# Kernel optimization log

Hardware: AMD Instinct MI355X
Metric: run time of the kernel (lower is better)

The kernel has to match this reference:

```python
import jax, jax.numpy as jnp
import numpy as np

B, T, C, HS = 32, 2048, 256, 64
LARGE_NEG = -1e9


def setup_inputs() -> dict:
    key = jax.random.key(0)
    k1, k2, k3, k4, k5 = jax.random.split(key, 5)
    q_input = jax.random.normal(k1, (B, T, C), dtype=jnp.float32)
    attn_mask = jax.random.randint(k2, (B, T), 0, 2) > 0  # (B, Tk) bool padding mask
    s = 1.0 / np.sqrt(C)  # ~ nn.Linear default init scale
    Wq = jax.random.normal(k3, (C, HS), dtype=jnp.float32) * s
    Wk = jax.random.normal(k4, (C, HS), dtype=jnp.float32) * s
    Wv = jax.random.normal(k5, (C, HS), dtype=jnp.float32) * s
    return {"q_input": q_input, "Wq": Wq, "Wk": Wk, "Wv": Wv, "attn_mask": attn_mask}


def reference(q_input, Wq, Wk, Wv, attn_mask):
    # self-attention: kv_input = q_input
    q = q_input @ Wq  # (B, Tq, HS)
    k = q_input @ Wk  # (B, Tk, HS)
    v = q_input @ Wv  # (B, Tk, HS)
    scale = HS ** -0.5
    w = jnp.einsum('bqd,bkd->bqk', q, k) * scale  # (B, Tq, Tk)
    causal = jnp.tril(jnp.ones((T, T), dtype=bool))  # tril buffer slice
    w = jnp.where(causal[None, :, :], w, LARGE_NEG)
    # (B, Tk) padding mask -> broadcast over query dim, matching unsqueeze(1)
    w = jnp.where(attn_mask[:, None, :], w, LARGE_NEG)
    w = jax.nn.softmax(w, axis=-1)
    # dropout is identity in eval mode (deterministic reference)
    out = jnp.einsum('bqk,bkd->bqd', w, v)  # (B, Tq, HS)
    return out
```

## Files before the change

kernel.cpp:

```cpp
#include <hip/hip_runtime.h>
#include <hip/hip_bf16.h>

#define NB 32
#define NT 2048
#define NC 256
#define NH 64
#define QB 64
#define KB 64
#define MT 128
#define KC 64

typedef __attribute__((ext_vector_type(8))) short bf16x8;
typedef __attribute__((ext_vector_type(4))) float f32x4;

static constexpr float SCALE2 = 0.18033688011112042f;
static constexpr float LNEG   = -1e9f;

static __device__ inline short f2b(float x) {
    __hip_bfloat16 h = __float2bfloat16(x);
    return *reinterpret_cast<short*>(&h);
}
static __device__ inline float b2f(short s) {
    unsigned int u = ((unsigned int)(unsigned short)s) << 16;
    float f; __builtin_memcpy(&f, &u, 4); return f;
}

static __device__ inline void dma16(const __hip_bfloat16* g, __hip_bfloat16* l) {
    __builtin_amdgcn_global_load_lds(
        (const __attribute__((address_space(1))) unsigned int*)g,
        (__attribute__((address_space(3))) unsigned int*)l, 16, 0, 0);
}

__global__ __launch_bounds__(256) void prep_kernel(
    const float* __restrict__ Wq, const float* __restrict__ Wk,
    const float* __restrict__ Wv, const int* __restrict__ M,
    __hip_bfloat16* __restrict__ Wt, float* __restrict__ Bias)
{
    const int n = blockIdx.x;
    if (n < 192) {
        const int k = threadIdx.x;
        const float* Wm = (n < 64) ? Wq : ((n < 128) ? Wk : Wv);
        Wt[n * NC + k] = __float2bfloat16(Wm[k * NH + (n & 63)]);
    } else {
        const int i = (n - 192) * 256 + threadIdx.x;
        Bias[i] = M[i] ? 0.f : LNEG;
    }
}

__global__ __launch_bounds__(256, 2) void qkv_kernel(
    const float* __restrict__ X, const __hip_bfloat16* __restrict__ Wt,
    __hip_bfloat16* __restrict__ Q, __hip_bfloat16* __restrict__ K,
    __hip_bfloat16* __restrict__ Vt)
{
    __shared__ __hip_bfloat16 x_lds[MT][KC + 8];
    __shared__ __hip_bfloat16 w_lds[192][KC + 8];

    const int row0 = blockIdx.x * MT;
    const int tid  = threadIdx.x;
    const int wid  = tid >> 6;
    const int lane = tid & 63;
    const int l15  = lane & 15;
    const int lg   = lane >> 4;

    f32x4 aQ[4][2], aK[4][2], aV[2][4];
    #pragma unroll
    for (int i = 0; i < 4; ++i)
        #pragma unroll
        for (int j = 0; j < 2; ++j) {
            aQ[i][j] = (f32x4){0.f,0.f,0.f,0.f};
            aK[i][j] = (f32x4){0.f,0.f,0.f,0.f};
            aV[j][i] = (f32x4){0.f,0.f,0.f,0.f};
        }

    float4 xp[4][2];
    bf16x8 wp[6];
    #pragma unroll
    for (int i = 0; i < 4; ++i) {
        int u = tid + i * 256;
        int r = u >> 3, c8 = (u & 7) * 8;
        const float* src = &X[(size_t)(row0 + r) * NC + c8];
        xp[i][0] = *(const float4*)(src);
        xp[i][1] = *(const float4*)(src + 4);
    }
    #pragma unroll
    for (int i = 0; i < 6; ++i) {
        int u = tid + i * 256;
        int r = u >> 3, c8 = (u & 7) * 8;
        wp[i] = *reinterpret_cast<const bf16x8*>(&Wt[r * NC + c8]);
    }

    for (int kc = 0; kc < NC / KC; ++kc) {
        __syncthreads();
        #pragma unroll
        for (int i = 0; i < 4; ++i) {
            int u = tid + i * 256;
            int r = u >> 3, c8 = (u & 7) * 8;
            bf16x8 o;
            o[0]=f2b(xp[i][0].x); o[1]=f2b(xp[i][0].y);
            o[2]=f2b(xp[i][0].z); o[3]=f2b(xp[i][0].w);
            o[4]=f2b(xp[i][1].x); o[5]=f2b(xp[i][1].y);
            o[6]=f2b(xp[i][1].z); o[7]=f2b(xp[i][1].w);
            *reinterpret_cast<bf16x8*>(&x_lds[r][c8]) = o;
        }
        #pragma unroll
        for (int i = 0; i < 6; ++i) {
            int u = tid + i * 256;
            int r = u >> 3, c8 = (u & 7) * 8;
            *reinterpret_cast<bf16x8*>(&w_lds[r][c8]) = wp[i];
        }
        __syncthreads();

        if (kc + 1 < NC / KC) {
            const int off = (kc + 1) * KC;
            #pragma unroll
            for (int i = 0; i < 4; ++i) {
                int u = tid + i * 256;
                int r = u >> 3, c8 = (u & 7) * 8;
                const float* src = &X[(size_t)(row0 + r) * NC + off + c8];
                xp[i][0] = *(const float4*)(src);
                xp[i][1] = *(const float4*)(src + 4);
            }
            #pragma unroll
            for (int i = 0; i < 6; ++i) {
                int u = tid + i * 256;
                int r = u >> 3, c8 = (u & 7) * 8;
                wp[i] = *reinterpret_cast<const bf16x8*>(&Wt[r * NC + off + c8]);
            }
        }

        #pragma unroll
        for (int ks = 0; ks < 2; ++ks) {
            bf16x8 xf[2];
            #pragma unroll
            for (int tf = 0; tf < 2; ++tf)
                xf[tf] = *reinterpret_cast<const bf16x8*>(
                    &x_lds[wid * 32 + tf * 16 + l15][ks * 32 + lg * 8]);
            #pragma unroll
            for (int nf = 0; nf < 4; ++nf) {
                bf16x8 wq = *reinterpret_cast<const bf16x8*>(
                    &w_lds[nf * 16 + l15][ks * 32 + lg * 8]);
                bf16x8 wk = *reinterpret_cast<const bf16x8*>(
                    &w_lds[64 + nf * 16 + l15][ks * 32 + lg * 8]);
                bf16x8 wv = *reinterpret_cast<const bf16x8*>(
                    &w_lds[128 + nf * 16 + l15][ks * 32 + lg * 8]);
                #pragma unroll
                for (int tf = 0; tf < 2; ++tf) {
                    aQ[nf][tf] = __builtin_amdgcn_mfma_f32_16x16x32_bf16(wq, xf[tf], aQ[nf][tf], 0, 0, 0);
                    aK[nf][tf] = __builtin_amdgcn_mfma_f32_16x16x32_bf16(wk, xf[tf], aK[nf][tf], 0, 0, 0);
                    aV[tf][nf] = __builtin_amdgcn_mfma_f32_16x16x32_bf16(xf[tf], wv, aV[tf][nf], 0, 0, 0);
                }
            }
        }
    }

    const int b  = row0 >> 11;
    const int t0 = row0 & (NT - 1);
    #pragma unroll
    for (int nf = 0; nf < 4; ++nf)
        #pragma unroll
        for (int tf = 0; tf < 2; ++tf) {
            size_t o = (size_t)(row0 + wid * 32 + tf * 16 + l15) * NH + nf * 16 + lg * 4;
            short4 sq, sk;
            sq.x = f2b(aQ[nf][tf][0] * SCALE2); sq.y = f2b(aQ[nf][tf][1] * SCALE2);
            sq.z = f2b(aQ[nf][tf][2] * SCALE2); sq.w = f2b(aQ[nf][tf][3] * SCALE2);
            sk.x = f2b(aK[nf][tf][0]); sk.y = f2b(aK[nf][tf][1]);
            sk.z = f2b(aK[nf][tf][2]); sk.w = f2b(aK[nf][tf][3]);
            *reinterpret_cast<short4*>(&Q[o]) = sq;
            *reinterpret_cast<short4*>(&K[o]) = sk;
        }
    #pragma unroll
    for (int tf = 0; tf < 2; ++tf)
        #pragma unroll
        for (int df = 0; df < 4; ++df) {
            int d  = df * 16 + l15;
            int t4 = t0 + wid * 32 + tf * 16 + lg * 4;
            short4 sv;
            sv.x = f2b(aV[tf][df][0]); sv.y = f2b(aV[tf][df][1]);
            sv.z = f2b(aV[tf][df][2]); sv.w = f2b(aV[tf][df][3]);
            *reinterpret_cast<short4*>(&Vt[((size_t)b * NH + d) * NT + t4]) = sv;
        }
}

__global__ __launch_bounds__(1024) void meanv_kernel(
    const __hip_bfloat16* __restrict__ Vt, float* __restrict__ MV)
{
    __shared__ float red[NH][17];
    const int b    = blockIdx.x;
    const int tid  = threadIdx.x;
    const int d    = tid >> 4;
    const int part = tid & 15;
    const __hip_bfloat16* row = Vt + ((size_t)b * NH + d) * NT;
    float s = 0.f;
    for (int t = part * 128; t < part * 128 + 128; t += 8) {
        bf16x8 v = *reinterpret_cast<const bf16x8*>(&row[t]);
        #pragma unroll
        for (int j = 0; j < 8; ++j) s += b2f(v[j]);
    }
    red[d][part] = s;
    __syncthreads();
    if (part == 0) {
        float tot = 0.f;
        #pragma unroll
        for (int i = 0; i < 16; ++i) tot += red[d][i];
        MV[b * NH + d] = tot * (1.0f / NT);
    }
}

template<bool CAUSAL>
static __device__ inline void sm_step(
    int q, int k0, const int (&koff)[4],
    const f32x4 (&s)[4], float& m_r, float& l_r,
    bool& resc, float& al, bf16x8& pb0, bf16x8& pb1)
{
    float y[4][4];
    #pragma unroll
    for (int jt = 0; jt < 4; ++jt)
        #pragma unroll
        for (int r = 0; r < 4; ++r) {
            float v = s[jt][r];
            if (CAUSAL && (k0 + koff[jt] + r > q)) v = LNEG;
            y[jt][r] = v;
        }
    float pmax = y[0][0];
    #pragma unroll
    for (int jt = 0; jt < 4; ++jt)
        #pragma unroll
        for (int r = 0; r < 4; ++r) pmax = fmaxf(pmax, y[jt][r]);

    resc = __any(pmax > m_r + 8.0f);
    al   = 1.0f;
    if (resc) {
        float tm = fmaxf(pmax, __shfl_xor(pmax, 16));
        tm = fmaxf(tm, __shfl_xor(tm, 32));
        const float mnew = fmaxf(m_r, tm);
        al  = __builtin_amdgcn_exp2f(m_r - mnew);
        m_r = mnew;
        l_r *= al;
    }

    float p[4][4], rs = 0.f;
    #pragma unroll
    for (int jt = 0; jt < 4; ++jt)
        #pragma unroll
        for (int r = 0; r < 4; ++r) {
            p[jt][r] = __builtin_amdgcn_exp2f(y[jt][r] - m_r);
            rs += p[jt][r];
        }
    l_r += rs;
    #pragma unroll
    for (int r = 0; r < 4; ++r) {
        pb0[r]     = f2b(p[0][r]);
        pb0[4 + r] = f2b(p[1][r]);
        pb1[r]     = f2b(p[2][r]);
        pb1[4 + r] = f2b(p[3][r]);
    }
}

__global__ __launch_bounds__(256) void attn_kernel(
    const __hip_bfloat16* __restrict__ Q, const __hip_bfloat16* __restrict__ K,
    const __hip_bfloat16* __restrict__ Vt, const float* __restrict__ Bias,
    const float* __restrict__ MV, float* __restrict__ Out)
{
    __shared__ __hip_bfloat16 k_lds[2][KB][NH];
    __shared__ __hip_bfloat16 vt_lds[2][NH][KB];

    const int bid  = blockIdx.x;
    const int xcd  = bid & 7;
    const int slot = bid >> 3;
    const int b    = xcd * 4 + (slot >> 4);
    const int pi   = slot & 15;
    const int gA   = pi, gB = 31 - pi;

    const int tid  = threadIdx.x;
    const int wid  = tid >> 6;
    const int lane = tid & 63;
    const int l15  = lane & 15;
    const int lg   = lane >> 4;

    const __hip_bfloat16* Kg = K  + (size_t)b * NT * NH;
    const __hip_bfloat16* Vg = Vt + (size_t)b * NH * NT;
    const float* Bb = Bias + b * NT;

    const int qA = gA * QB + wid * 16 + l15;
    const int qB = gB * QB + wid * 16 + l15;
    bf16x8 qA0, qA1, qB0, qB1;
    {
        const __hip_bfloat16* Qr = Q + ((size_t)b * NT + qA) * NH;
        qA0 = *reinterpret_cast<const bf16x8*>(&Qr[lg * 8]);
        qA1 = *reinterpret_cast<const bf16x8*>(&Qr[lg * 8 + 32]);
        const __hip_bfloat16* Qs = Q + ((size_t)b * NT + qB) * NH;
        qB0 = *reinterpret_cast<const bf16x8*>(&Qs[lg * 8]);
        qB1 = *reinterpret_cast<const bf16x8*>(&Qs[lg * 8 + 32]);
    }

    f32x4 oA[4], oB[4];
    #pragma unroll
    for (int dt = 0; dt < 4; ++dt) {
        oA[dt] = (f32x4){0.f,0.f,0.f,0.f};
        oB[dt] = (f32x4){0.f,0.f,0.f,0.f};
    }
    float mA = -3.0e38f, lA = 0.f, mB = -3.0e38f, lB = 0.f;

    int kr[4], koff[4];
    #pragma unroll
    for (int jt = 0; jt < 4; ++jt) {
        kr[jt]   = ((jt & 2) << 4) | ((l15 >> 2) << 3) | ((jt & 1) << 2) | (l15 & 3);
        koff[jt] = ((jt & 2) << 4) | (lg << 3) | ((jt & 1) << 2);
    }
    const int swk  = (l15 & 3) | (((l15 >> 2) & 1) << 2);
    const int swv  = (l15 & 3) | (((l15 >> 3) & 1) << 2);
    const int kch0 = ((lg ^ swk) & 7) * 8;
    const int vch0 = ((lg ^ swv) & 7) * 8;

    int srowL[2], schL[2];
    #pragma unroll
    for (int i = 0; i < 2; ++i) {
        const int ci  = wid * 2 + i;
        srowL[i] = ci * 8 + (lane >> 3);
        const int sw = ((lane >> 3) & 3) | ((ci & 1) << 2);
        schL[i]  = ((lane & 7) ^ sw) * 8;
    }

    #define STAGE(buf, kt_) do {                                              \
        const int _k0 = (kt_) * KB;                                           \
        _Pragma("unroll")                                                     \
        for (int i = 0; i < 2; ++i) {                                         \
            dma16(Kg + (size_t)(_k0 + srowL[i]) * NH + schL[i],               \
                  &k_lds[buf][(wid * 2 + i) * 8][0]);                         \
            dma16(Vg + (size_t)srowL[i] * NT + _k0 + schL[i],                 \
                  &vt_lds[buf][(wid * 2 + i) * 8][0]);                        \
        }                                                                     \
    } while (0)

    STAGE(0, 0);
    int cur = 0;

    f32x4 bias_cur[4], bias_nxt[4];
    #pragma unroll
    for (int jt = 0; jt < 4; ++jt)
        bias_cur[jt] = *reinterpret_cast<const f32x4*>(&Bb[koff[jt]]);

    for (int kt = 0; kt <= gB; ++kt) {
        asm volatile("s_waitcnt vmcnt(0)" ::: "memory");
        __syncthreads();
        if (kt < gB) {
            STAGE(cur ^ 1, kt + 1);
            const int kn = (kt + 1) * KB;
            #pragma unroll
            for (int jt = 0; jt < 4; ++jt)
                bias_nxt[jt] = *reinterpret_cast<const f32x4*>(&Bb[kn + koff[jt]]);
        }

        const int k0   = kt * KB;
        const bool aAct = (kt <= gA);

        f32x4 sA[4], sB[4];
        __builtin_amdgcn_s_setprio(1);
        #pragma unroll
        for (int jt = 0; jt < 4; ++jt) {
            bf16x8 kfa = *reinterpret_cast<const bf16x8*>(&k_lds[cur][kr[jt]][kch0]);
            bf16x8 kfb = *reinterpret_cast<const bf16x8*>(&k_lds[cur][kr[jt]][kch0 ^ 32]);
            sB[jt] = __builtin_amdgcn_mfma_f32_16x16x32_bf16(kfa, qB0, bias_cur[jt], 0, 0, 0);
            sB[jt] = __builtin_amdgcn_mfma_f32_16x16x32_bf16(kfb, qB1, sB[jt], 0, 0, 0);
            if (aAct) {
                sA[jt] = __builtin_amdgcn_mfma_f32_16x16x32_bf16(kfa, qA0, bias_cur[jt], 0, 0, 0);
                sA[jt] = __builtin_amdgcn_mfma_f32_16x16x32_bf16(kfb, qA1, sA[jt], 0, 0, 0);
            }
        }
        __builtin_amdgcn_s_setprio(0);

        bool rescA = false, rescB = false;
        float alA = 1.f, alB = 1.f;
        bf16x8 pA0, pA1, pB0, pB1;
        if (kt == gB) sm_step<true >(qB, k0, koff, sB, mB, lB, rescB, alB, pB0, pB1);
        else          sm_step<false>(qB, k0, koff, sB, mB, lB, rescB, alB, pB0, pB1);
        if (aAct) {
            if (kt == gA) sm_step<true >(qA, k0, koff, sA, mA, lA, rescA, alA, pA0, pA1);
            else          sm_step<false>(qA, k0, koff, sA, mA, lA, rescA, alA, pA0, pA1);
        }

        if (rescB) {
            #pragma unroll
            for (int dt = 0; dt < 4; ++dt)
                #pragma unroll
                for (int r = 0; r < 4; ++r) oB[dt][r] *= alB;
        }
        if (rescA) {
            #pragma unroll
            for (int dt = 0; dt < 4; ++dt)
                #pragma unroll
                for (int r = 0; r < 4; ++r) oA[dt][r] *= alA;
        }

        __builtin_amdgcn_s_setprio(1);
        #pragma unroll
        for (int dt = 0; dt < 4; ++dt) {
            bf16x8 vfa = *reinterpret_cast<const bf16x8*>(&vt_lds[cur][dt * 16 + l15][vch0]);
            bf16x8 vfb = *reinterpret_cast<const bf16x8*>(&vt_lds[cur][dt * 16 + l15][vch0 ^ 32]);
            oB[dt] = __builtin_amdgcn_mfma_f32_16x16x32_bf16(vfa, pB0, oB[dt], 0, 0, 0);
            oB[dt] = __builtin_amdgcn_mfma_f32_16x16x32_bf16(vfb, pB1, oB[dt], 0, 0, 0);
            if (aAct) {
                oA[dt] = __builtin_amdgcn_mfma_f32_16x16x32_bf16(vfa, pA0, oA[dt], 0, 0, 0);
                oA[dt] = __builtin_amdgcn_mfma_f32_16x16x32_bf16(vfb, pA1, oA[dt], 0, 0, 0);
            }
        }
        __builtin_amdgcn_s_setprio(0);

        #pragma unroll
        for (int jt = 0; jt < 4; ++jt) bias_cur[jt] = bias_nxt[jt];
        cur ^= 1;
    }
    #undef STAGE

    float lAt = lA + __shfl_xor(lA, 16); lAt += __shfl_xor(lAt, 32);
    float lBt = lB + __shfl_xor(lB, 16); lBt += __shfl_xor(lBt, 32);

    #pragma unroll
    for (int grp = 0; grp < 2; ++grp) {
        const int   q  = grp ? qB : qA;
        const float m  = grp ? mB : mA;
        const float l  = grp ? lBt : lAt;
        const f32x4* o = grp ? oB : oA;
        const bool degen = (m <= -5.0e8f);
        const float inv  = degen ? 0.f : 1.0f / l;
        float* Or = Out + ((size_t)b * NT + q) * NH;
        #pragma unroll
        for (int dt = 0; dt < 4; ++dt) {
            float4 ov;
            if (degen) {
                ov = *reinterpret_cast<const float4*>(&MV[b * NH + dt * 16 + lg * 4]);
            } else {
                ov.x = o[dt][0] * inv; ov.y = o[dt][1] * inv;
                ov.z = o[dt][2] * inv; ov.w = o[dt][3] * inv;
            }
            *reinterpret_cast<float4*>(&Or[dt * 16 + lg * 4]) = ov;
        }
    }
}

extern "C" void kernel_launch(void* const* d_in, const int* in_sizes, int n_in,
                              void* d_out, int out_size, void* d_ws, size_t ws_size,
                              hipStream_t stream)
{
    const float* X  = (const float*)d_in[0];
    const float* Wq = (const float*)d_in[1];
    const float* Wk = (const float*)d_in[2];
    const float* Wv = (const float*)d_in[3];
    const int*   M  = (const int*)d_in[4];
    float* out = (float*)d_out;

    __hip_bfloat16* Qp = (__hip_bfloat16*)d_ws;
    __hip_bfloat16* Kp = Qp + (size_t)NB * NT * NH;
    __hip_bfloat16* Vp = Kp + (size_t)NB * NT * NH;
    float* MVp = (float*)(Vp + (size_t)NB * NT * NH);
    __hip_bfloat16* Wtp = (__hip_bfloat16*)(MVp + NB * NH);
    float* Biasp = (float*)(Wtp + 192 * NC);

    prep_kernel<<<448, 256, 0, stream>>>(Wq, Wk, Wv, M, Wtp, Biasp);
    qkv_kernel<<<NB * NT / MT, 256, 0, stream>>>(X, Wtp, Qp, Kp, Vp);
    meanv_kernel<<<NB, 1024, 0, stream>>>(Vp, MVp);
    attn_kernel<<<512, 256, 0, stream>>>(Qp, Kp, Vp, Biasp, MVp, out);
}
```

Measured before the change: 85.49 us.

## Split paired causal query tiles into one tile per block, doubling grid

Each attention block previously processed two query tiles (pi and 31-pi) so that causal work was balanced and K/V tiles loaded into LDS were shared by both. Now each block handles a single 64-row query tile, the grid doubles to 1024 blocks ordered from the longest tiles down, and launch bounds request 4 blocks per CU. This lowers register pressure and raises occupancy. In exchange, K/V LDS staging is no longer shared between two tiles, and the longest-first ordering is now what balances the uneven causal work.

Measured after the change: 89.28 us. 4.4% more time.

```diff
diff --git a/kernel.cpp b/kernel.cpp
--- a/kernel.cpp
+++ b/kernel.cpp
@@ -256,7 +256,7 @@
     }
 }
 
-__global__ __launch_bounds__(256) void attn_kernel(
+__global__ __launch_bounds__(256, 4) void attn_kernel(
     const __hip_bfloat16* __restrict__ Q, const __hip_bfloat16* __restrict__ K,
     const __hip_bfloat16* __restrict__ Vt, const float* __restrict__ Bias,
     const float* __restrict__ MV, float* __restrict__ Out)
@@ -267,9 +267,8 @@
     const int bid  = blockIdx.x;
     const int xcd  = bid & 7;
     const int slot = bid >> 3;
-    const int b    = xcd * 4 + (slot >> 4);
-    const int pi   = slot & 15;
-    const int gA   = pi, gB = 31 - pi;
+    const int b    = xcd * 4 + (slot >> 5);
+    const int qg   = 31 - (slot & 31);
 
     const int tid  = threadIdx.x;
     const int wid  = tid >> 6;
@@ -281,25 +280,18 @@
     const __hip_bfloat16* Vg = Vt + (size_t)b * NH * NT;
     const float* Bb = Bias + b * NT;
 
-    const int qA = gA * QB + wid * 16 + l15;
-    const int qB = gB * QB + wid * 16 + l15;
-    bf16x8 qA0, qA1, qB0, qB1;
+    const int q = qg * QB + wid * 16 + l15;
+    bf16x8 qf0, qf1;
     {
-        const __hip_bfloat16* Qr = Q + ((size_t)b * NT + qA) * NH;
-        qA0 = *reinterpret_cast<const bf16x8*>(&Qr[lg * 8]);
-        qA1 = *reinterpret_cast<const bf16x8*>(&Qr[lg * 8 + 32]);
-        const __hip_bfloat16* Qs = Q + ((size_t)b * NT + qB) * NH;
-        qB0 = *reinterpret_cast<const bf16x8*>(&Qs[lg * 8]);
-        qB1 = *reinterpret_cast<const bf16x8*>(&Qs[lg * 8 + 32]);
-    }
-
-    f32x4 oA[4], oB[4];
-    #pragma unroll
-    for (int dt = 0; dt < 4; ++dt) {
-        oA[dt] = (f32x4){0.f,0.f,0.f,0.f};
-        oB[dt] = (f32x4){0.f,0.f,0.f,0.f};
-    }
-    float mA = -3.0e38f, lA = 0.f, mB = -3.0e38f, lB = 0.f;
+        const __hip_bfloat16* Qr = Q + ((size_t)b * NT + q) * NH;
+        qf0 = *reinterpret_cast<const bf16x8*>(&Qr[lg * 8]);
+        qf1 = *reinterpret_cast<const bf16x8*>(&Qr[lg * 8 + 32]);
+    }
+
+    f32x4 o_acc[4];
+    #pragma unroll
+    for (int dt = 0; dt < 4; ++dt) o_acc[dt] = (f32x4){0.f,0.f,0.f,0.f};
+    float m_r = -3.0e38f, l_r = 0.f;
 
     int kr[4], koff[4];
     #pragma unroll
@@ -340,10 +332,10 @@
     for (int jt = 0; jt < 4; ++jt)
         bias_cur[jt] = *reinterpret_cast<const f32x4*>(&Bb[koff[jt]]);
 
-    for (int kt = 0; kt <= gB; ++kt) {
+    for (int kt = 0; kt <= qg; ++kt) {
         asm volatile("s_waitcnt vmcnt(0)" ::: "memory");
         __syncthreads();
-        if (kt < gB) {
+        if (kt < qg) {
             STAGE(cur ^ 1, kt + 1);
             const int kn = (kt + 1) * KB;
             #pragma unroll
@@ -351,45 +343,30 @@
                 bias_nxt[jt] = *reinterpret_cast<const f32x4*>(&Bb[kn + koff[jt]]);
         }
 
-        const int k0   = kt * KB;
-        const bool aAct = (kt <= gA);
-
-        f32x4 sA[4], sB[4];
+        const int k0 = kt * KB;
+
+        f32x4 s[4];
         __builtin_amdgcn_s_setprio(1);
         #pragma unroll
         for (int jt = 0; jt < 4; ++jt) {
             bf16x8 kfa = *reinterpret_cast<const bf16x8*>(&k_lds[cur][kr[jt]][kch0]);
             bf16x8 kfb = *reinterpret_cast<const bf16x8*>(&k_lds[cur][kr[jt]][kch0 ^ 32]);
-            sB[jt] = __builtin_amdgcn_mfma_f32_16x16x32_bf16(kfa, qB0, bias_cur[jt], 0, 0, 0);
-            sB[jt] = __builtin_amdgcn_mfma_f32_16x16x32_bf16(kfb, qB1, sB[jt], 0, 0, 0);
-            if (aAct) {
-                sA[jt] = __builtin_amdgcn_mfma_f32_16x16x32_bf16(kfa, qA0, bias_cur[jt], 0, 0, 0);
-                sA[jt] = __builtin_amdgcn_mfma_f32_16x16x32_bf16(kfb, qA1, sA[jt], 0, 0, 0);
-            }
+            s[jt] = __builtin_amdgcn_mfma_f32_16x16x32_bf16(kfa, qf0, bias_cur[jt], 0, 0, 0);
+            s[jt] = __builtin_amdgcn_mfma_f32_16x16x32_bf16(kfb, qf1, s[jt], 0, 0, 0);
         }
         __builtin_amdgcn_s_setprio(0);
 
-        bool rescA = false, rescB = false;
-        float alA = 1.f, alB = 1.f;
-        bf16x8 pA0, pA1, pB0, pB1;
-        if (kt == gB) sm_step<true >(qB, k0, koff, sB, mB, lB, rescB, alB, pB0, pB1);
-        else          sm_step<false>(qB, k0, koff, sB, mB, lB, rescB, alB, pB0, pB1);
-        if (aAct) {
-            if (kt == gA) sm_step<true >(qA, k0, koff, sA, mA, lA, rescA, alA, pA0, pA1);
-            else          sm_step<false>(qA, k0, koff, sA, mA, lA, rescA, alA, pA0, pA1);
-        }
-
-        if (rescB) {
+        bool resc = false;
+        float al = 1.f;
+        bf16x8 pb0, pb1;
+        if (kt == qg) sm_step<true >(q, k0, koff, s, m_r, l_r, resc, al, pb0, pb1);
+        else          sm_step<false>(q, k0, koff, s, m_r, l_r, resc, al, pb0, pb1);
+
+        if (resc) {
             #pragma unroll
             for (int dt = 0; dt < 4; ++dt)
                 #pragma unroll
-                for (int r = 0; r < 4; ++r) oB[dt][r] *= alB;
-        }
-        if (rescA) {
-            #pragma unroll
-            for (int dt = 0; dt < 4; ++dt)
-                #pragma unroll
-                for (int r = 0; r < 4; ++r) oA[dt][r] *= alA;
+                for (int r = 0; r < 4; ++r) o_acc[dt][r] *= al;
         }
 
         __builtin_amdgcn_s_setprio(1);
@@ -397,12 +374,8 @@
         for (int dt = 0; dt < 4; ++dt) {
             bf16x8 vfa = *reinterpret_cast<const bf16x8*>(&vt_lds[cur][dt * 16 + l15][vch0]);
             bf16x8 vfb = *reinterpret_cast<const bf16x8*>(&vt_lds[cur][dt * 16 + l15][vch0 ^ 32]);
-            oB[dt] = __builtin_amdgcn_mfma_f32_16x16x32_bf16(vfa, pB0, oB[dt], 0, 0, 0);
-            oB[dt] = __builtin_amdgcn_mfma_f32_16x16x32_bf16(vfb, pB1, oB[dt], 0, 0, 0);
-            if (aAct) {
-                oA[dt] = __builtin_amdgcn_mfma_f32_16x16x32_bf16(vfa, pA0, oA[dt], 0, 0, 0);
-                oA[dt] = __builtin_amdgcn_mfma_f32_16x16x32_bf16(vfb, pA1, oA[dt], 0, 0, 0);
-            }
+            o_acc[dt] = __builtin_amdgcn_mfma_f32_16x16x32_bf16(vfa, pb0, o_acc[dt], 0, 0, 0);
+            o_acc[dt] = __builtin_amdgcn_mfma_f32_16x16x32_bf16(vfb, pb1, o_acc[dt], 0, 0, 0);
         }
         __builtin_amdgcn_s_setprio(0);
 
@@ -412,29 +385,21 @@
     }
     #undef STAGE
 
-    float lAt = lA + __shfl_xor(lA, 16); lAt += __shfl_xor(lAt, 32);
-    float lBt = lB + __shfl_xor(lB, 16); lBt += __shfl_xor(lBt, 32);
-
-    #pragma unroll
-    for (int grp = 0; grp < 2; ++grp) {
-        const int   q  = grp ? qB : qA;
-        const float m  = grp ? mB : mA;
-        const float l  = grp ? lBt : lAt;
-        const f32x4* o = grp ? oB : oA;
-        const bool degen = (m <= -5.0e8f);
-        const float inv  = degen ? 0.f : 1.0f / l;
-        float* Or = Out + ((size_t)b * NT + q) * NH;
-        #pragma unroll
-        for (int dt = 0; dt < 4; ++dt) {
-            float4 ov;
-            if (degen) {
-                ov = *reinterpret_cast<const float4*>(&MV[b * NH + dt * 16 + lg * 4]);
-            } else {
-                ov.x = o[dt][0] * inv; ov.y = o[dt][1] * inv;
-                ov.z = o[dt][2] * inv; ov.w = o[dt][3] * inv;
-            }
-            *reinterpret_cast<float4*>(&Or[dt * 16 + lg * 4]) = ov;
-        }
+    float lt = l_r + __shfl_xor(l_r, 16); lt += __shfl_xor(lt, 32);
+
+    const bool degen = (m_r <= -5.0e8f);
+    const float inv  = degen ? 0.f : 1.0f / lt;
+    float* Or = Out + ((size_t)b * NT + q) * NH;
+    #pragma unroll
+    for (int dt = 0; dt < 4; ++dt) {
+        float4 ov;
+        if (degen) {
+            ov = *reinterpret_cast<const float4*>(&MV[b * NH + dt * 16 + lg * 4]);
+        } else {
+            ov.x = o_acc[dt][0] * inv; ov.y = o_acc[dt][1] * inv;
+            ov.z = o_acc[dt][2] * inv; ov.w = o_acc[dt][3] * inv;
+        }
+        *reinterpret_cast<float4*>(&Or[dt * 16 + lg * 4]) = ov;
     }
 }
 
@@ -459,5 +424,5 @@
     prep_kernel<<<448, 256, 0, stream>>>(Wq, Wk, Wv, M, Wtp, Biasp);
     qkv_kernel<<<NB * NT / MT, 256, 0, stream>>>(X, Wtp, Qp, Kp, Vp);
     meanv_kernel<<<NB, 1024, 0, stream>>>(Vp, MVp);
-    attn_kernel<<<512, 256, 0, stream>>>(Qp, Kp, Vp, Biasp, MVp, out);
-}
+    attn_kernel<<<1024, 256, 0, stream>>>(Qp, Kp, Vp, Biasp, MVp, out);
+}
```

## Fuse mean-of-V reduction into QKV kernel via atomics; drop bias prefetch

Applied to the files above, without the earlier changes.

Removes the separate meanv kernel launch. The per-batch mean of V is now accumulated in the QKV projection epilogue, using fp32 accumulators, wave shuffles and atomicAdd into a buffer that prep_kernel zeroes in an extra block. The attention loop also stops double-buffering the bias registers and loads the bias for the current tile directly, which lowers register pressure but exposes that load's latency. Atomics make the mean's summation order nondeterministic, and it is now taken over fp32 values instead of rounded bf16.

Result: faster. 75.78 us (-11.4%).

```diff
diff --git a/kernel.cpp b/kernel.cpp
--- a/kernel.cpp
+++ b/kernel.cpp
@@ -34,23 +34,27 @@
 __global__ __launch_bounds__(256) void prep_kernel(
     const float* __restrict__ Wq, const float* __restrict__ Wk,
     const float* __restrict__ Wv, const int* __restrict__ M,
-    __hip_bfloat16* __restrict__ Wt, float* __restrict__ Bias)
+    __hip_bfloat16* __restrict__ Wt, float* __restrict__ Bias,
+    float* __restrict__ MV)
 {
     const int n = blockIdx.x;
     if (n < 192) {
         const int k = threadIdx.x;
         const float* Wm = (n < 64) ? Wq : ((n < 128) ? Wk : Wv);
         Wt[n * NC + k] = __float2bfloat16(Wm[k * NH + (n & 63)]);
-    } else {
+    } else if (n < 448) {
         const int i = (n - 192) * 256 + threadIdx.x;
         Bias[i] = M[i] ? 0.f : LNEG;
+    } else {
+        #pragma unroll
+        for (int j = 0; j < 8; ++j) MV[threadIdx.x * 8 + j] = 0.f;
     }
 }
 
 __global__ __launch_bounds__(256, 2) void qkv_kernel(
     const float* __restrict__ X, const __hip_bfloat16* __restrict__ Wt,
     __hip_bfloat16* __restrict__ Q, __hip_bfloat16* __restrict__ K,
-    __hip_bfloat16* __restrict__ Vt)
+    __hip_bfloat16* __restrict__ Vt, float* __restrict__ MV)
 {
     __shared__ __hip_bfloat16 x_lds[MT][KC + 8];
     __shared__ __hip_bfloat16 w_lds[192][KC + 8];
@@ -179,30 +183,18 @@
             sv.z = f2b(aV[tf][df][2]); sv.w = f2b(aV[tf][df][3]);
             *reinterpret_cast<short4*>(&Vt[((size_t)b * NH + d) * NT + t4]) = sv;
         }
-}
-
-__global__ __launch_bounds__(1024) void meanv_kernel(
-    const __hip_bfloat16* __restrict__ Vt, float* __restrict__ MV)
-{
-    __shared__ float red[NH][17];
-    const int b    = blockIdx.x;
-    const int tid  = threadIdx.x;
-    const int d    = tid >> 4;
-    const int part = tid & 15;
-    const __hip_bfloat16* row = Vt + ((size_t)b * NH + d) * NT;
-    float s = 0.f;
-    for (int t = part * 128; t < part * 128 + 128; t += 8) {
-        bf16x8 v = *reinterpret_cast<const bf16x8*>(&row[t]);
-        #pragma unroll
-        for (int j = 0; j < 8; ++j) s += b2f(v[j]);
-    }
-    red[d][part] = s;
-    __syncthreads();
-    if (part == 0) {
-        float tot = 0.f;
-        #pragma unroll
-        for (int i = 0; i < 16; ++i) tot += red[d][i];
-        MV[b * NH + d] = tot * (1.0f / NT);
+
+    #pragma unroll
+    for (int df = 0; df < 4; ++df) {
+        float s = 0.f;
+        #pragma unroll
+        for (int tf = 0; tf < 2; ++tf)
+            #pragma unroll
+            for (int r = 0; r < 4; ++r) s += aV[tf][df][r];
+        s += __shfl_xor(s, 16);
+        s += __shfl_xor(s, 32);
+        if (lg == 0)
+            atomicAdd(&MV[b * NH + df * 16 + l15], s * (1.0f / NT));
     }
 }
 
@@ -335,24 +327,18 @@
     STAGE(0, 0);
     int cur = 0;
 
-    f32x4 bias_cur[4], bias_nxt[4];
-    #pragma unroll
-    for (int jt = 0; jt < 4; ++jt)
-        bias_cur[jt] = *reinterpret_cast<const f32x4*>(&Bb[koff[jt]]);
-
     for (int kt = 0; kt <= gB; ++kt) {
+        const int k0 = kt * KB;
         asm volatile("s_waitcnt vmcnt(0)" ::: "memory");
         __syncthreads();
-        if (kt < gB) {
-            STAGE(cur ^ 1, kt + 1);
-            const int kn = (kt + 1) * KB;
-            #pragma unroll
-            for (int jt = 0; jt < 4; ++jt)
-                bias_nxt[jt] = *reinterpret_cast<const f32x4*>(&Bb[kn + koff[jt]]);
-        }
-
-        const int k0   = kt * KB;
+        if (kt < gB) STAGE(cur ^ 1, kt + 1);
+
         const bool aAct = (kt <= gA);
+
+        f32x4 bias4[4];
+        #pragma unroll
+        for (int jt = 0; jt < 4; ++jt)
+            bias4[jt] = *reinterpret_cast<const f32x4*>(&Bb[k0 + koff[jt]]);
 
         f32x4 sA[4], sB[4];
         __builtin_amdgcn_s_setprio(1);
@@ -360,10 +346,10 @@
         for (int jt = 0; jt < 4; ++jt) {
             bf16x8 kfa = *reinterpret_cast<const bf16x8*>(&k_lds[cur][kr[jt]][kch0]);
             bf16x8 kfb = *reinterpret_cast<const bf16x8*>(&k_lds[cur][kr[jt]][kch0 ^ 32]);
-            sB[jt] = __builtin_amdgcn_mfma_f32_16x16x32_bf16(kfa, qB0, bias_cur[jt], 0, 0, 0);
+            sB[jt] = __builtin_amdgcn_mfma_f32_16x16x32_bf16(kfa, qB0, bias4[jt], 0, 0, 0);
             sB[jt] = __builtin_amdgcn_mfma_f32_16x16x32_bf16(kfb, qB1, sB[jt], 0, 0, 0);
             if (aAct) {
-                sA[jt] = __builtin_amdgcn_mfma_f32_16x16x32_bf16(kfa, qA0, bias_cur[jt], 0, 0, 0);
+                sA[jt] = __builtin_amdgcn_mfma_f32_16x16x32_bf16(kfa, qA0, bias4[jt], 0, 0, 0);
                 sA[jt] = __builtin_amdgcn_mfma_f32_16x16x32_bf16(kfb, qA1, sA[jt], 0, 0, 0);
             }
         }
@@ -405,9 +391,6 @@
             }
         }
         __builtin_amdgcn_s_setprio(0);
-
-        #pragma unroll
-        for (int jt = 0; jt < 4; ++jt) bias_cur[jt] = bias_nxt[jt];
         cur ^= 1;
     }
     #undef STAGE
@@ -456,8 +439,7 @@
     __hip_bfloat16* Wtp = (__hip_bfloat16*)(MVp + NB * NH);
     float* Biasp = (float*)(Wtp + 192 * NC);
 
-    prep_kernel<<<448, 256, 0, stream>>>(Wq, Wk, Wv, M, Wtp, Biasp);
-    qkv_kernel<<<NB * NT / MT, 256, 0, stream>>>(X, Wtp, Qp, Kp, Vp);
-    meanv_kernel<<<NB, 1024, 0, stream>>>(Vp, MVp);
+    prep_kernel<<<449, 256, 0, stream>>>(Wq, Wk, Wv, M, Wtp, Biasp, MVp);
+    qkv_kernel<<<NB * NT / MT, 256, 0, stream>>>(X, Wtp, Qp, Kp, Vp, MVp);
     attn_kernel<<<512, 256, 0, stream>>>(Qp, Kp, Vp, Biasp, MVp, out);
 }
```
